# Kernel tuning notes

Measured on AMD Instinct MI355X. Metric: run time of the kernel, lower is better.

Reference implementation:

```python
import jax, jax.numpy as jnp
import numpy as np

B, C, T, R = 32, 8, 512, 256


def setup_inputs() -> dict:
    key = jax.random.key(0)
    k1, k2, k3 = jax.random.split(key, 3)
    x = jax.random.normal(k1, (B, C, T), dtype=jnp.float32)
    # W_in ~ U(-1, 1), shape [reservoir, input_size=1]
    W_in = jax.random.uniform(k2, (R, 1), minval=-1.0, maxval=1.0, dtype=jnp.float32)
    # diagonal of W_res ~ U(-1, 1)
    d = jax.random.uniform(k3, (R,), minval=-1.0, maxval=1.0, dtype=jnp.float32)
    return {"x": x, "W_in": W_in, "d": d}


def reference(x, W_in, d):
    # state_{t} = tanh(u_t * W_in[:,0] + state_{t-1} * d), vectorized over (B,C)
    w = W_in[:, 0]                       # [R]
    b, c, t = x.shape
    xs = jnp.moveaxis(x, -1, 0)          # [T, B, C]
    init = jnp.zeros((b, c, w.shape[0]), dtype=x.dtype)  # [B, C, R]

    def step(state, u_t):
        s = jnp.tanh(u_t[..., None] * w + state * d)  # [B, C, R]
        return s, s

    _, states = jax.lax.scan(step, init, xs)  # [T, B, C, R]
    return jnp.moveaxis(states, 0, 2)         # [B, C, T, R]
```

## Files before the change

kernel.cpp:

```cpp
#include <hip/hip_runtime.h>


constexpr int Bdim = 32;
constexpr int Cdim = 8;
constexpr int Tdim = 512;
constexpr int Rdim = 256;
constexpr int T4   = Tdim / 4;

__device__ __forceinline__ float tanh_p(float z) {
    float p = fmaf(z, -2.76076847742355e-16f, 2.00018790482477e-13f);
    p = fmaf(z, p, -8.60467152213735e-11f);
    p = fmaf(z, p, 5.12229709037114e-08f);
    p = fmaf(z, p, 1.48572235717979e-05f * 0.0f + 1.48572235717979e-05f);
    p = fmaf(z, p, 6.37261928875436e-04f);
    p = fmaf(z, p, 4.89352455891786e-03f);
    return p;
}
__device__ __forceinline__ float tanh_q(float z) {
    float q = fmaf(z, 1.19825839466702e-06f, 1.18534705686654e-04f);
    q = fmaf(z, q, 2.26843463243900e-03f);
    q = fmaf(z, q, 4.89352518554385e-03f);
    return q;
}

__global__ __launch_bounds__(256, 1) void esn_scan_kernel(
    const float* __restrict__ x,
    const float* __restrict__ W_in,
    const float* __restrict__ d,
    float* __restrict__ out)
{
    const int bc = blockIdx.x;
    const int r  = threadIdx.x;

    const float wc = W_in[r];
    const float dc = d[r];

    __shared__ float4 xs4[T4];
    {
        const float4* __restrict__ x4 = reinterpret_cast<const float4*>(x + bc * Tdim);
        if (r < T4) xs4[r] = x4[r];
    }
    __syncthreads();

    float* __restrict__ o = out + (size_t)bc * Tdim * Rdim + r;

    float4 a0 = xs4[0], a1 = xs4[1];
    float4 b0 = xs4[2], b1 = xs4[3];

    float a = a0.x * wc;

    #pragma unroll 1
    for (int g = 0; g < Tdim / 8; ++g) {
        int pf = 2 * g + 4; if (pf > T4 - 2) pf = T4 - 2;
        float4 c0 = xs4[pf], c1 = xs4[pf + 1];

        float pre[8];
        pre[0] = a0.y * wc;
        pre[1] = a0.z * wc;
        pre[2] = a0.w * wc;
        pre[3] = a1.x * wc;
        pre[4] = a1.y * wc;
        pre[5] = a1.z * wc;
        pre[6] = a1.w * wc;
        pre[7] = b0.x * wc;

        float* ob  = o + (size_t)(g * 8) * Rdim;
        float* ob4 = ob + (size_t)4 * Rdim;

        #pragma unroll
        for (int j = 0; j < 8; ++j) {
            float z  = a * a;
            float p  = tanh_p(z);
            float q  = tanh_q(z);
            float rc = __builtin_amdgcn_rcpf(q);
            float pa = p * a;
            float s  = pa * rc;
            if (j < 4) ob[j * Rdim] = s;
            else       ob4[(j - 4) * Rdim] = s;
            a = fmaf(pa * dc, rc, pre[j]);
            a = fminf(7.90531f, fmaxf(-7.90531f, a));
        }

        a0 = b0; a1 = b1;
        b0 = c0; b1 = c1;
    }
}

extern "C" void kernel_launch(void* const* d_in, const int* in_sizes, int n_in,
                              void* d_out, int out_size, void* d_ws, size_t ws_size,
                              hipStream_t stream) {
    const float* x    = (const float*)d_in[0];
    const float* W_in = (const float*)d_in[1];
    const float* d    = (const float*)d_in[2];
    float* out        = (float*)d_out;

    dim3 grid(Bdim * Cdim);
    dim3 block(Rdim);
    esn_scan_kernel<<<grid, block, 0, stream>>>(x, W_in, d, out);
}
```

Baseline: 31.93 us.

## Replace rational tanh with exp2-based form and split stores across duplicated blocks

Rewrites the tanh recurrence as tanh(a)=1-2/(exp(2a)+1), using hardware exp2 and rcp with scaling constants folded into the weights. The serial dependency chain per step shrinks from a long polynomial to an exp, an add, a rcp and an fma. The grid is doubled so two blocks each recompute the full scan for the same (b,c), with each block writing only alternating timesteps. This doubles the compute but halves the stores per block and raises occupancy. The clamp is gone, so overflow of exp2 must be handled by rcp(inf)=0.

```diff
diff --git a/kernel.cpp b/kernel.cpp
--- a/kernel.cpp
+++ b/kernel.cpp
@@ -7,33 +7,32 @@
 constexpr int Rdim = 256;
 constexpr int T4   = Tdim / 4;
 
-__device__ __forceinline__ float tanh_p(float z) {
-    float p = fmaf(z, -2.76076847742355e-16f, 2.00018790482477e-13f);
-    p = fmaf(z, p, -8.60467152213735e-11f);
-    p = fmaf(z, p, 5.12229709037114e-08f);
-    p = fmaf(z, p, 1.48572235717979e-05f * 0.0f + 1.48572235717979e-05f);
-    p = fmaf(z, p, 6.37261928875436e-04f);
-    p = fmaf(z, p, 4.89352455891786e-03f);
-    return p;
-}
-__device__ __forceinline__ float tanh_q(float z) {
-    float q = fmaf(z, 1.19825839466702e-06f, 1.18534705686654e-04f);
-    q = fmaf(z, q, 2.26843463243900e-03f);
-    q = fmaf(z, q, 4.89352518554385e-03f);
-    return q;
+__device__ __forceinline__ float fast_exp2(float v) {
+#if defined(__has_builtin)
+#if __has_builtin(__builtin_amdgcn_exp2f)
+    return __builtin_amdgcn_exp2f(v);
+#else
+    return exp2f(v);
+#endif
+#else
+    return exp2f(v);
+#endif
 }
 
-__global__ __launch_bounds__(256, 1) void esn_scan_kernel(
+__global__ __launch_bounds__(256, 2) void esn_scan_kernel(
     const float* __restrict__ x,
     const float* __restrict__ W_in,
     const float* __restrict__ d,
     float* __restrict__ out)
 {
-    const int bc = blockIdx.x;
-    const int r  = threadIdx.x;
+    const int bc    = blockIdx.x;
+    const int phase = blockIdx.y;
+    const int r     = threadIdx.x;
 
-    const float wc = W_in[r];
-    const float dc = d[r];
+    const float K    = 2.0f * 1.4426950408889634f;
+    const float wk   = W_in[r] * K;
+    const float dk   = d[r] * K;
+    const float m2dk = -2.0f * dk;
 
     __shared__ float4 xs4[T4];
     {
@@ -47,7 +46,7 @@
     float4 a0 = xs4[0], a1 = xs4[1];
     float4 b0 = xs4[2], b1 = xs4[3];
 
-    float a = a0.x * wc;
+    float earg = a0.x * wk;
 
     #pragma unroll 1
     for (int g = 0; g < Tdim / 8; ++g) {
@@ -55,30 +54,35 @@
         float4 c0 = xs4[pf], c1 = xs4[pf + 1];
 
         float pre[8];
-        pre[0] = a0.y * wc;
-        pre[1] = a0.z * wc;
-        pre[2] = a0.w * wc;
-        pre[3] = a1.x * wc;
-        pre[4] = a1.y * wc;
-        pre[5] = a1.z * wc;
-        pre[6] = a1.w * wc;
-        pre[7] = b0.x * wc;
+        pre[0] = fmaf(a0.y, wk, dk);
+        pre[1] = fmaf(a0.z, wk, dk);
+        pre[2] = fmaf(a0.w, wk, dk);
+        pre[3] = fmaf(a1.x, wk, dk);
+        pre[4] = fmaf(a1.y, wk, dk);
+        pre[5] = fmaf(a1.z, wk, dk);
+        pre[6] = fmaf(a1.w, wk, dk);
+        pre[7] = fmaf(b0.x, wk, dk);
 
-        float* ob  = o + (size_t)(g * 8) * Rdim;
-        float* ob4 = ob + (size_t)4 * Rdim;
-
+        float sv[8];
         #pragma unroll
         for (int j = 0; j < 8; ++j) {
-            float z  = a * a;
-            float p  = tanh_p(z);
-            float q  = tanh_q(z);
-            float rc = __builtin_amdgcn_rcpf(q);
-            float pa = p * a;
-            float s  = pa * rc;
-            if (j < 4) ob[j * Rdim] = s;
-            else       ob4[(j - 4) * Rdim] = s;
-            a = fmaf(pa * dc, rc, pre[j]);
-            a = fminf(7.90531f, fmaxf(-7.90531f, a));
+            float e  = fast_exp2(earg);
+            float rc = __builtin_amdgcn_rcpf(e + 1.0f);
+            sv[j] = fmaf(-2.0f, rc, 1.0f);
+            earg  = fmaf(m2dk, rc, pre[j]);
+        }
+
+        float* ob = o + (size_t)(g * 8) * Rdim;
+        if (phase == 0) {
+            ob[0 * Rdim] = sv[0];
+            ob[2 * Rdim] = sv[2];
+            ob[4 * Rdim] = sv[4];
+            ob[6 * Rdim] = sv[6];
+        } else {
+            ob[1 * Rdim] = sv[1];
+            ob[3 * Rdim] = sv[3];
+            ob[5 * Rdim] = sv[5];
+            ob[7 * Rdim] = sv[7];
         }
 
         a0 = b0; a1 = b1;
@@ -94,7 +98,7 @@
     const float* d    = (const float*)d_in[2];
     float* out        = (float*)d_out;
 
-    dim3 grid(Bdim * Cdim);
+    dim3 grid(Bdim * Cdim, 2);
     dim3 block(Rdim);
     esn_scan_kernel<<<grid, block, 0, stream>>>(x, W_in, d, out);
 }
```

Measured after the change: 28.64 us. -10.3%, faster.
